# Optimization experiments

Hardware: AMD Instinct MI355X
Metric: run time of the kernel (lower is better)

Reference implementation:

```python
import jax, jax.numpy as jnp
import numpy as np

B, N, C, K1, K2, TD = 4, 4096, 128, 16, 8, 64
CIN = 2 * (3 + C)  # 262


def setup_inputs() -> dict:
    key = jax.random.key(0)
    ks = jax.random.split(key, 8)
    s = 0.05
    feature = jax.random.normal(ks[0], (B, C, N), jnp.float32)
    xyz = jax.random.normal(ks[1], (B, 3, N), jnp.float32)
    wq = jax.random.normal(ks[2], (TD, CIN), jnp.float32) * s
    wk = jax.random.normal(ks[3], (TD, CIN), jnp.float32) * s
    wv = jax.random.normal(ks[4], (TD, CIN), jnp.float32) * s
    w1 = jax.random.normal(ks[5], (C, TD), jnp.float32) * s
    bq = jnp.zeros((TD,), jnp.float32)
    bk = jnp.zeros((TD,), jnp.float32)
    bv = jnp.zeros((TD,), jnp.float32)
    b1 = jnp.zeros((C,), jnp.float32)
    return {"feature": feature, "xyz": xyz, "wq": wq, "bq": bq,
            "wk": wk, "bk": bk, "wv": wv, "bv": bv, "w1": w1, "b1": b1}


def _group(x, ind):
    # x: [B, Cx, N], ind: [B, N, K] -> [B, Cx, K, N]; g[b,c,k,n] = x[b,c,ind[b,n,k]]
    g = jnp.take_along_axis(x[:, :, None, :], ind[:, None, :, :], axis=3)  # [B,Cx,N,K]
    return g.transpose(0, 1, 3, 2)


def reference(feature, xyz, wq, bq, wk, bk, wv, bv, w1, b1):
    # --- KNN (self-included then dropped), idx[b,n,k] = k-th nearest of point n ---
    sq = jnp.sum(xyz * xyz, axis=1)                                   # [B,N]
    dist = sq[:, :, None] + sq[:, None, :] - 2.0 * jnp.einsum('bdn,bdm->bnm', xyz, xyz)
    _, idx = jax.lax.top_k(-dist, K1 + 1)                             # [B,N,17]
    idx = idx[:, :, 1:]                                               # drop self -> [B,N,16]
    idx1 = idx[:, :, :K2]                                             # [B,N,8]

    gxyz = _group(xyz, idx)        # [B,3,16,N]
    gxyz1 = _group(xyz, idx1)      # [B,3,8,N]
    gfea = _group(feature, idx)    # [B,C,16,N]
    gfea1 = _group(feature, idx1)  # [B,C,8,N]

    rel_xyz = gxyz - xyz[:, :, None, :]
    rel_xyz1 = gxyz1 - xyz[:, :, None, :]
    rel_fea = gfea - feature[:, :, None, :]
    rel_fea1 = gfea1 - feature[:, :, None, :]

    def relpos(rx, rf, K):
        return jnp.concatenate([
            rx,
            jnp.broadcast_to(xyz[:, :, None, :], (B, 3, K, N)),
            rf,
            jnp.broadcast_to(feature[:, :, None, :], (B, C, K, N)),
        ], axis=1)  # [B,262,K,N]

    rel_pos = relpos(rel_xyz, rel_fea, K1)     # [B,262,16,N]
    rel_pos1 = relpos(rel_xyz1, rel_fea1, K2)  # [B,262,8,N]

    # 1x1 Conv2d projections
    q = jnp.einsum('oc,bckn->bokn', wq, rel_pos1) + bq[None, :, None, None]  # [B,64,8,N]
    k = jnp.einsum('oc,bckn->bokn', wk, rel_pos) + bk[None, :, None, None]   # [B,64,16,N]
    v = jnp.einsum('oc,bckn->bokn', wv, rel_pos) + bv[None, :, None, None]   # [B,64,16,N]

    attn = jnp.einsum('bmnf,bmjf->bnjf', q, k)   # [B,8,16,N]
    attn = jax.nn.softmax(attn, axis=-2)         # softmax over j (16 neighbors)
    res = jnp.einsum('bnjf,bmjf->bmf', attn, v)  # [B,64,N]

    out = jnp.einsum('om,bmf->bof', w1, res) + b1[None, :, None]  # Conv1d 64->128
    return out + feature
```

## Files before the change

kernel.cpp:

```cpp
#include <hip/hip_runtime.h>

#define NN 4096
#define CCH 128

__global__ __launch_bounds__(256) void transpose_w(
    const float* __restrict__ wq, const float* __restrict__ wk, const float* __restrict__ wv,
    const float* __restrict__ w1, const float* __restrict__ xyz,
    float* __restrict__ wTq, float* __restrict__ wTk, float* __restrict__ wTv,
    float* __restrict__ w1T, float* __restrict__ wPack, float4* __restrict__ pts4) {
  int t = blockIdx.x * 256 + threadIdx.x;
  if (t < 64 * 262) {
    int o = t / 262, c = t - o * 262;
    wTq[c * 64 + o] = wq[t];
    wTk[c * 64 + o] = wk[t];
    wTv[c * 64 + o] = wv[t];
  }
  if (t < 128 * 64) {
    int r = t >> 6, c2 = t & 63;
    w1T[c2 * 128 + r] = w1[t];
  }
  if (t < 49152) {
    int r = t & 3, o = (t >> 2) & 63;
    int g = t >> 8;
    int ct = g / 6, mh = g - ct * 6;
    int m = mh >> 1, h = mh & 1;
    const float* wsrc = (m == 0) ? wq : ((m == 1) ? wk : wv);
    wPack[t] = wsrc[o * 262 + (h ? 134 : 6) + 4 * ct + r];
  }
  if (t < 4 * NN) {
    int bb = t >> 12, i = t & 4095;
    const float* xb = xyz + (size_t)bb * 3 * NN;
    float x = xb[i], y = xb[NN + i], z = xb[2 * NN + i];
    pts4[t] = make_float4(x, y, z, x * x + y * y + z * z);
  }
}

__global__ __launch_bounds__(1024, 4) void knn_kernel(const float4* __restrict__ pts4,
                                                      int* __restrict__ idxout) {
  __shared__ float bufA[64 * 64];
  __shared__ float bufB[64 * 64];
  __shared__ unsigned long long hits[32 * 64];
  __shared__ int cnt[64];
  const int b  = blockIdx.x >> 6;
  const int n0 = (blockIdx.x & 63) << 6;
  const int ql = threadIdx.x & 63;
  const int ch = __builtin_amdgcn_readfirstlane(threadIdx.x >> 6);
  if (threadIdx.x < 64) cnt[threadIdx.x] = 0;
  const int q = n0 + ql;
  const float4* pb4 = pts4 + ((size_t)b << 12);
  const float4 me = pb4[q];
  float bd0 = 3.0e38f, bd1 = 3.0e38f, bd2 = 3.0e38f, bd3 = 3.0e38f;
  const int m0 = ch << 8;
  for (int mb = m0; mb < m0 + 256; mb += 8) {
    float4 P[8];
#pragma unroll
    for (int u = 0; u < 8; ++u) P[u] = pb4[mb + u];
#pragma unroll
    for (int u = 0; u < 8; ++u) {
      float d = me.w + P[u].w - 2.0f * (me.x * P[u].x + me.y * P[u].y + me.z * P[u].z);
      d = (mb + u == q) ? 3.0e38f : d;
      bd3 = __builtin_amdgcn_fmed3f(d, bd2, bd3);
      bd2 = __builtin_amdgcn_fmed3f(d, bd1, bd2);
      bd1 = __builtin_amdgcn_fmed3f(d, bd0, bd1);
      bd0 = fminf(bd0, d);
    }
  }
  {
    const int r0 = (ch * 4) * 64 + ql;
    bufA[r0] = bd0; bufA[r0 + 64] = bd1; bufA[r0 + 128] = bd2; bufA[r0 + 192] = bd3;
  }
  __syncthreads();
  if (ch < 8) {
    const int a0 = (2 * ch) * 4, b0 = (2 * ch + 1) * 4;
    float o8[8]; int pa = 0, pb = 0;
#pragma unroll
    for (int k = 0; k < 8; ++k) {
      float va = (pa < 4) ? bufA[(a0 + pa) * 64 + ql] : 3.0e38f;
      float vb = (pb < 4) ? bufA[(b0 + pb) * 64 + ql] : 3.0e38f;
      bool ta = va <= vb;
      o8[k] = ta ? va : vb;
      pa += ta ? 1 : 0; pb += ta ? 0 : 1;
    }
#pragma unroll
    for (int k = 0; k < 8; ++k) bufB[(ch * 8 + k) * 64 + ql] = o8[k];
  }
  __syncthreads();
  if (ch < 4) {
    const int a0 = (2 * ch) * 8, b0 = (2 * ch + 1) * 8;
    float o16[16]; int pa = 0, pb = 0;
#pragma unroll
    for (int k = 0; k < 16; ++k) {
      float va = (pa < 8) ? bufB[(a0 + pa) * 64 + ql] : 3.0e38f;
      float vb = (pb < 8) ? bufB[(b0 + pb) * 64 + ql] : 3.0e38f;
      bool ta = va <= vb;
      o16[k] = ta ? va : vb;
      pa += ta ? 1 : 0; pb += ta ? 0 : 1;
    }
#pragma unroll
    for (int k = 0; k < 16; ++k) bufA[(ch * 16 + k) * 64 + ql] = o16[k];
  }
  __syncthreads();
  if (ch < 2) {
    const int a0 = (2 * ch) * 16, b0 = (2 * ch + 1) * 16;
    float o16[16]; int pa = 0, pb = 0;
#pragma unroll
    for (int k = 0; k < 16; ++k) {
      float va = bufA[(a0 + pa) * 64 + ql];
      float vb = bufA[(b0 + pb) * 64 + ql];
      bool ta = va <= vb;
      o16[k] = ta ? va : vb;
      pa += ta ? 1 : 0; pb += ta ? 0 : 1;
    }
#pragma unroll
    for (int k = 0; k < 16; ++k) bufB[(ch * 16 + k) * 64 + ql] = o16[k];
  }
  __syncthreads();
  if (ch == 0) {
    float v = 0.f; int pa = 0, pb = 0;
#pragma unroll
    for (int k = 0; k < 16; ++k) {
      float va = bufB[pa * 64 + ql];
      float vb = bufB[(16 + pb) * 64 + ql];
      bool ta = va <= vb;
      v = ta ? va : vb;
      pa += ta ? 1 : 0; pb += ta ? 0 : 1;
    }
    bufA[15 * 64 + ql] = v;
  }
  __syncthreads();
  const float tau = bufA[15 * 64 + ql];
  for (int mb = m0; mb < m0 + 256; mb += 8) {
    float4 P[8];
#pragma unroll
    for (int u = 0; u < 8; ++u) P[u] = pb4[mb + u];
#pragma unroll
    for (int u = 0; u < 8; ++u) {
      float d = me.w + P[u].w - 2.0f * (me.x * P[u].x + me.y * P[u].y + me.z * P[u].z);
      if (d <= tau && (mb + u) != q) {
        int pos = atomicAdd(&cnt[ql], 1);
        if (pos < 32) {
          unsigned int f = __float_as_uint(d);
          f ^= (f >> 31) ? 0xFFFFFFFFu : 0x80000000u;
          hits[pos * 64 + ql] = ((unsigned long long)f << 32) | (unsigned int)(mb + u);
        }
      }
    }
  }
  __syncthreads();
  const int l5 = threadIdx.x & 31;
#pragma unroll
  for (int t = 0; t < 2; ++t) {
    const int qq = (t * 1024 + (int)threadIdx.x) >> 5;
    int nv = cnt[qq]; nv = nv > 32 ? 32 : nv;
    unsigned long long key = (l5 < nv) ? hits[l5 * 64 + qq] : ~0ULL;
#pragma unroll
    for (int k = 2; k <= 32; k <<= 1) {
#pragma unroll
      for (int jm = k >> 1; jm > 0; jm >>= 1) {
        unsigned long long o2 = __shfl_xor(key, jm, 32);
        bool asc = ((l5 & k) == 0);
        bool lower = ((l5 & jm) == 0);
        unsigned long long mn = key < o2 ? key : o2;
        unsigned long long mx = key < o2 ? o2 : key;
        key = (lower == asc) ? mn : mx;
      }
    }
    if (l5 < 16)
      idxout[((size_t)((b << 12) + n0 + qq)) * 16 + l5] = (int)(key & 0xFFFFFFFFu);
  }
}

__global__ __launch_bounds__(512) void proj_kernel(
    const float* __restrict__ feature, const float* __restrict__ xyz,
    const float* __restrict__ wTq, const float* __restrict__ wTk, const float* __restrict__ wTv,
    const float* __restrict__ wPack,
    const float* __restrict__ bq, const float* __restrict__ bk, const float* __restrict__ bv,
    float* __restrict__ uq, float* __restrict__ cq,
    float* __restrict__ uk, float* __restrict__ ck,
    float* __restrict__ uv, float* __restrict__ cv) {
  __shared__ float fl[64][132];
  __shared__ float4 wl[2 * 32 * 64];
  const int p0 = blockIdx.x << 6;
  const int b  = p0 >> 12;
  const int n0 = p0 & 4095;
  {
    const int i  = threadIdx.x & 63;
    const int c0 = threadIdx.x >> 6;
    const float* fb = feature + (size_t)b * CCH * NN + n0 + i;
    for (int cc = c0; cc < CCH; cc += 8) fl[i][cc] = fb[(size_t)cc * NN];
    if (threadIdx.x < 192) {
      const int d = threadIdx.x >> 6;
      fl[i][128 + d] = xyz[((size_t)b * 3 + d) * NN + n0 + i];
    }
  }
  const int o  = threadIdx.x & 63;
  const int pg = threadIdx.x >> 6;
  const float4* wp = reinterpret_cast<const float4*>(wPack);

  for (int m = 0; m < 3; ++m) {
    __syncthreads();
    for (int d4 = threadIdx.x; d4 < 4096; d4 += 512) {
      const int h = d4 >> 11, ct = (d4 >> 6) & 31, oo = d4 & 63;
      wl[d4] = wp[(ct * 6 + m * 2 + h) * 64 + oo];
    }
    __syncthreads();
    float aU[8], aT[8];
#pragma unroll
    for (int s = 0; s < 8; ++s) { aU[s] = 0.f; aT[s] = 0.f; }
    for (int ct = 0; ct < 32; ++ct) {
      const float4 wu = wl[ct * 64 + o];
      const float4 wt = wl[2048 + ct * 64 + o];
#pragma unroll
      for (int s = 0; s < 8; ++s) {
        const float4 f4 = *reinterpret_cast<const float4*>(&fl[pg * 8 + s][4 * ct]);
        aU[s] += wu.x * f4.x + wu.y * f4.y + wu.z * f4.z + wu.w * f4.w;
        aT[s] += wt.x * f4.x + wt.y * f4.y + wt.z * f4.z + wt.w * f4.w;
      }
    }
    const float* wtm = (m == 0) ? wTq : ((m == 1) ? wTk : wTv);
    float wxu[3], wxt[3];
#pragma unroll
    for (int dd = 0; dd < 3; ++dd) { wxu[dd] = wtm[dd * 64 + o]; wxt[dd] = wtm[(3 + dd) * 64 + o]; }
    const float bo = ((m == 0) ? bq : ((m == 1) ? bk : bv))[o];
    float* um = (m == 0) ? uq : ((m == 1) ? uk : uv);
    float* cm = (m == 0) ? cq : ((m == 1) ? ck : cv);
#pragma unroll
    for (int s = 0; s < 8; ++s) {
      const int p = pg * 8 + s;
      const float x = fl[p][128], y = fl[p][129], z = fl[p][130];
      const size_t gp = ((size_t)(p0 + p)) * 64 + o;
      const float uu = aU[s] + wxu[0] * x + wxu[1] * y + wxu[2] * z;
      const float tt = aT[s] + wxt[0] * x + wxt[1] * y + wxt[2] * z;
      um[gp] = uu; cm[gp] = tt + bo - uu;
    }
  }
}

__global__ __launch_bounds__(256) void attn_core(
    const int* __restrict__ idx,
    const float* __restrict__ uq, const float* __restrict__ cq,
    const float* __restrict__ uk, const float* __restrict__ ck,
    const float* __restrict__ uv, const float* __restrict__ cv,
    float* __restrict__ res_ws) {
  __shared__ float kq[4][24][68];
  const int slot = threadIdx.x >> 6;
  const int o    = threadIdx.x & 63;
  const int p = (blockIdx.x << 2) + slot;
  const int b = p >> 12;
  const int myidx = idx[(size_t)p * 16 + (o & 15)];
  const size_t pb = (size_t)p * 64 + o;
  const float cqo = cq[pb], cko = ck[pb], cvo = cv[pb];
  const int rowbase = (b << 12) * 64;
  float v[16];
#pragma unroll
  for (int j = 0; j < 16; ++j) {
    int nb = __shfl(myidx, j);
    int row = rowbase + nb * 64 + o;
    kq[slot][j][o] = uk[row] + cko;
    v[j] = uv[row] + cvo;
    if (j < 8) kq[slot][16 + j][o] = uq[row] + cqo;
  }
  const int i  = o >> 3;
  const int jj = o & 7;
  const float* qrow = &kq[slot][16 + i][0];
  const float* k0r  = &kq[slot][jj][0];
  const float* k1r  = &kq[slot][8 + jj][0];
  float s0 = 0.f, s1 = 0.f;
#pragma unroll
  for (int t = 0; t < 16; ++t) {
    float4 q4 = *reinterpret_cast<const float4*>(qrow + 4 * t);
    float4 a4 = *reinterpret_cast<const float4*>(k0r + 4 * t);
    float4 c4 = *reinterpret_cast<const float4*>(k1r + 4 * t);
    s0 += q4.x * a4.x + q4.y * a4.y + q4.z * a4.z + q4.w * a4.w;
    s1 += q4.x * c4.x + q4.y * c4.y + q4.z * c4.z + q4.w * c4.w;
  }
  float mx = fmaxf(s0, s1);
  mx = fmaxf(mx, __shfl_xor(mx, 1));
  mx = fmaxf(mx, __shfl_xor(mx, 2));
  mx = fmaxf(mx, __shfl_xor(mx, 4));
  float e0 = __expf(s0 - mx), e1 = __expf(s1 - mx);
  float den = e0 + e1;
  den += __shfl_xor(den, 1);
  den += __shfl_xor(den, 2);
  den += __shfl_xor(den, 4);
  const float inv = 1.0f / den;
  float w0 = e0 * inv, w1s = e1 * inv;
  w0 += __shfl_xor(w0, 8);   w1s += __shfl_xor(w1s, 8);
  w0 += __shfl_xor(w0, 16);  w1s += __shfl_xor(w1s, 16);
  w0 += __shfl_xor(w0, 32);  w1s += __shfl_xor(w1s, 32);
  float res = 0.f;
#pragma unroll
  for (int j = 0; j < 8; ++j) {
    res += __shfl(w0, j)  * v[j];
    res += __shfl(w1s, j) * v[j + 8];
  }
  res_ws[pb] = res;
}

__global__ __launch_bounds__(256) void out_kernel(
    const float* __restrict__ feature, const float* __restrict__ res,
    const float* __restrict__ w1T, const float* __restrict__ b1,
    float* __restrict__ out) {
  __shared__ float rT[64][66];
  const int p0 = blockIdx.x << 6;
  const int b  = p0 >> 12;
  const int n0 = p0 & 4095;
  {
    const int o = threadIdx.x & 63;
    for (int pp = threadIdx.x >> 6; pp < 64; pp += 4)
      rT[o][pp] = res[(size_t)(p0 + pp) * 64 + o];
  }
  __syncthreads();
  const int n = threadIdx.x & 63;
  const int c0 = (threadIdx.x >> 6) * 32;
  float acc[32];
#pragma unroll
  for (int cc = 0; cc < 32; ++cc) acc[cc] = b1[c0 + cc];
  for (int o = 0; o < 64; ++o) {
    const float rr = rT[o][n];
    const float* wrow = &w1T[o * 128 + c0];
#pragma unroll
    for (int cc = 0; cc < 32; ++cc) acc[cc] += wrow[cc] * rr;
  }
#pragma unroll
  for (int cc = 0; cc < 32; ++cc) {
    const size_t gi = ((size_t)(b * 128 + c0 + cc) << 12) + n0 + n;
    out[gi] = acc[cc] + feature[gi];
  }
}

extern "C" void kernel_launch(void* const* d_in, const int* in_sizes, int n_in,
                              void* d_out, int out_size, void* d_ws, size_t ws_size,
                              hipStream_t stream) {
  const float* feature = (const float*)d_in[0];
  const float* xyz     = (const float*)d_in[1];
  const float* wq      = (const float*)d_in[2];
  const float* bq      = (const float*)d_in[3];
  const float* wk      = (const float*)d_in[4];
  const float* bk      = (const float*)d_in[5];
  const float* wv      = (const float*)d_in[6];
  const float* bv      = (const float*)d_in[7];
  const float* w1      = (const float*)d_in[8];
  const float* b1      = (const float*)d_in[9];
  float* out = (float*)d_out;

  char* ws = (char*)d_ws;
  int*    idx  = (int*)ws;
  float4* pts4 = (float4*)(ws + (1u << 20));
  float* uq  = (float*)(ws + (2u << 20));
  float* cq  = uq + (1u << 20);
  float* uk  = cq + (1u << 20);
  float* ck  = uk + (1u << 20);
  float* uv  = ck + (1u << 20);
  float* cv  = uv + (1u << 20);
  float* res = cv + (1u << 20);
  float* wTq = res + (1u << 20);
  float* wTk = wTq + 262 * 64;
  float* wTv = wTk + 262 * 64;
  float* w1T = wTv + 262 * 64;
  float* wPk = w1T + 128 * 64;

  transpose_w<<<192, 256, 0, stream>>>(wq, wk, wv, w1, xyz, wTq, wTk, wTv, w1T, wPk, pts4);
  knn_kernel<<<256, 1024, 0, stream>>>(pts4, idx);
  proj_kernel<<<256, 512, 0, stream>>>(feature, xyz, wTq, wTk, wTv, wPk, bq, bk, bv,
                                       uq, cq, uk, ck, uv, cv);
  attn_core<<<4096, 256, 0, stream>>>(idx, uq, cq, uk, ck, uv, cv, res);
  out_kernel<<<256, 256, 0, stream>>>(feature, res, w1T, b1, out);
}
```

Measured before the change: 228.8 us.

## Split KNN search across two blocks per query tile and merge results

The KNN kernel now runs two blocks per 64-query tile, each scanning half of the candidate points, so twice as many blocks are launched to fill the GPU's compute units. Each half writes sorted 64-bit distance/index keys to workspace, and a new merge kernel combines the two sorted lists into the final 16 indices. The shared-memory hits array is padded to stride 65 to reduce bank conflicts, and the output kernel uses 512 threads with 16 accumulators each. The cost is an extra kernel launch plus a workspace round trip for the keys. The keys buffer reuses the uq region, which is only written after the merge.

Measured after the change: 218.6 us. 4.4% less time.

```diff
diff --git a/kernel.cpp b/kernel.cpp
--- a/kernel.cpp
+++ b/kernel.cpp
@@ -35,14 +35,16 @@
   }
 }
 
-__global__ __launch_bounds__(1024, 4) void knn_kernel(const float4* __restrict__ pts4,
-                                                      int* __restrict__ idxout) {
+__global__ __launch_bounds__(1024, 4) void knn_half(const float4* __restrict__ pts4,
+                                                    unsigned long long* __restrict__ keys_ws) {
   __shared__ float bufA[64 * 64];
   __shared__ float bufB[64 * 64];
-  __shared__ unsigned long long hits[32 * 64];
+  __shared__ unsigned long long hits[32 * 65];
   __shared__ int cnt[64];
-  const int b  = blockIdx.x >> 6;
-  const int n0 = (blockIdx.x & 63) << 6;
+  const int b  = blockIdx.x >> 7;
+  const int g  = (blockIdx.x >> 1) & 63;
+  const int h  = blockIdx.x & 1;
+  const int n0 = g << 6;
   const int ql = threadIdx.x & 63;
   const int ch = __builtin_amdgcn_readfirstlane(threadIdx.x >> 6);
   if (threadIdx.x < 64) cnt[threadIdx.x] = 0;
@@ -50,8 +52,8 @@
   const float4* pb4 = pts4 + ((size_t)b << 12);
   const float4 me = pb4[q];
   float bd0 = 3.0e38f, bd1 = 3.0e38f, bd2 = 3.0e38f, bd3 = 3.0e38f;
-  const int m0 = ch << 8;
-  for (int mb = m0; mb < m0 + 256; mb += 8) {
+  const int m0 = (h << 11) + (ch << 7);
+  for (int mb = m0; mb < m0 + 128; mb += 8) {
     float4 P[8];
 #pragma unroll
     for (int u = 0; u < 8; ++u) P[u] = pb4[mb + u];
@@ -129,7 +131,7 @@
   }
   __syncthreads();
   const float tau = bufA[15 * 64 + ql];
-  for (int mb = m0; mb < m0 + 256; mb += 8) {
+  for (int mb = m0; mb < m0 + 128; mb += 8) {
     float4 P[8];
 #pragma unroll
     for (int u = 0; u < 8; ++u) P[u] = pb4[mb + u];
@@ -141,7 +143,7 @@
         if (pos < 32) {
           unsigned int f = __float_as_uint(d);
           f ^= (f >> 31) ? 0xFFFFFFFFu : 0x80000000u;
-          hits[pos * 64 + ql] = ((unsigned long long)f << 32) | (unsigned int)(mb + u);
+          hits[pos * 65 + ql] = ((unsigned long long)f << 32) | (unsigned int)(mb + u);
         }
       }
     }
@@ -152,7 +154,7 @@
   for (int t = 0; t < 2; ++t) {
     const int qq = (t * 1024 + (int)threadIdx.x) >> 5;
     int nv = cnt[qq]; nv = nv > 32 ? 32 : nv;
-    unsigned long long key = (l5 < nv) ? hits[l5 * 64 + qq] : ~0ULL;
+    unsigned long long key = (l5 < nv) ? hits[l5 * 65 + qq] : ~0ULL;
 #pragma unroll
     for (int k = 2; k <= 32; k <<= 1) {
 #pragma unroll
@@ -165,8 +167,26 @@
         key = (lower == asc) ? mn : mx;
       }
     }
-    if (l5 < 16)
-      idxout[((size_t)((b << 12) + n0 + qq)) * 16 + l5] = (int)(key & 0xFFFFFFFFu);
+    if (l5 < 16) {
+      const size_t gq = (size_t)((b << 12) + n0 + qq);
+      keys_ws[((size_t)h << 18) + gq * 16 + l5] = key;
+    }
+  }
+}
+
+__global__ __launch_bounds__(256) void knn_merge(const unsigned long long* __restrict__ keys_ws,
+                                                 int* __restrict__ idxout) {
+  const int gq = blockIdx.x * 256 + threadIdx.x;
+  const unsigned long long* A  = keys_ws + (size_t)gq * 16;
+  const unsigned long long* Bp = keys_ws + (1u << 18) + (size_t)gq * 16;
+  int* op = idxout + (size_t)gq * 16;
+  int pa = 0, pb = 0;
+#pragma unroll
+  for (int k = 0; k < 16; ++k) {
+    unsigned long long va = A[pa], vb = Bp[pb];
+    bool ta = va <= vb;
+    op[k] = (int)((ta ? va : vb) & 0xFFFFFFFFu);
+    pa += ta ? 1 : 0; pb += ta ? 0 : 1;
   }
 }
 
@@ -297,7 +317,7 @@
   res_ws[pb] = res;
 }
 
-__global__ __launch_bounds__(256) void out_kernel(
+__global__ __launch_bounds__(512) void out_kernel(
     const float* __restrict__ feature, const float* __restrict__ res,
     const float* __restrict__ w1T, const float* __restrict__ b1,
     float* __restrict__ out) {
@@ -307,23 +327,23 @@
   const int n0 = p0 & 4095;
   {
     const int o = threadIdx.x & 63;
-    for (int pp = threadIdx.x >> 6; pp < 64; pp += 4)
+    for (int pp = threadIdx.x >> 6; pp < 64; pp += 8)
       rT[o][pp] = res[(size_t)(p0 + pp) * 64 + o];
   }
   __syncthreads();
   const int n = threadIdx.x & 63;
-  const int c0 = (threadIdx.x >> 6) * 32;
-  float acc[32];
-#pragma unroll
-  for (int cc = 0; cc < 32; ++cc) acc[cc] = b1[c0 + cc];
+  const int c0 = (threadIdx.x >> 6) * 16;
+  float acc[16];
+#pragma unroll
+  for (int cc = 0; cc < 16; ++cc) acc[cc] = b1[c0 + cc];
   for (int o = 0; o < 64; ++o) {
     const float rr = rT[o][n];
     const float* wrow = &w1T[o * 128 + c0];
 #pragma unroll
-    for (int cc = 0; cc < 32; ++cc) acc[cc] += wrow[cc] * rr;
-  }
-#pragma unroll
-  for (int cc = 0; cc < 32; ++cc) {
+    for (int cc = 0; cc < 16; ++cc) acc[cc] += wrow[cc] * rr;
+  }
+#pragma unroll
+  for (int cc = 0; cc < 16; ++cc) {
     const size_t gi = ((size_t)(b * 128 + c0 + cc) << 12) + n0 + n;
     out[gi] = acc[cc] + feature[gi];
   }
@@ -359,11 +379,13 @@
   float* wTv = wTk + 262 * 64;
   float* w1T = wTv + 262 * 64;
   float* wPk = w1T + 128 * 64;
+  unsigned long long* keys = (unsigned long long*)(ws + (2u << 20));
 
   transpose_w<<<192, 256, 0, stream>>>(wq, wk, wv, w1, xyz, wTq, wTk, wTv, w1T, wPk, pts4);
-  knn_kernel<<<256, 1024, 0, stream>>>(pts4, idx);
+  knn_half<<<512, 1024, 0, stream>>>(pts4, keys);
+  knn_merge<<<64, 256, 0, stream>>>(keys, idx);
   proj_kernel<<<256, 512, 0, stream>>>(feature, xyz, wTq, wTk, wTv, wPk, bq, bk, bv,
                                        uq, cq, uk, ck, uv, cv);
   attn_core<<<4096, 256, 0, stream>>>(idx, uq, cq, uk, ck, uv, cv, res);
-  out_kernel<<<256, 256, 0, stream>>>(feature, res, w1T, b1, out);
-}
+  out_kernel<<<256, 512, 0, stream>>>(feature, res, w1T, b1, out);
+}
```
